# Kernel optimization log

Measured on AMD Instinct MI355X. Metric: run time of the kernel, lower is better.

The kernel has to match this reference:

```python
import jax, jax.numpy as jnp
import numpy as np

KE = 14.3996
ALPHA = 0.3
CUTOFF = 10.0
K_MAX = 6
N_ATOMS = 100000
N_PAIRS = 6400000
N_MOL = 64


def _generate_kvecs():
    kr = np.arange(0, K_MAX + 1, dtype=np.float32)
    kr = np.concatenate([kr, -kr[1:]])
    # cartesian product of (kr, kr, kr)
    g = np.stack(np.meshgrid(kr, kr, kr, indexing='ij'), axis=-1).reshape(-1, 3)
    norm = (g ** 2).sum(axis=1)
    mask = (norm <= K_MAX ** 2 + 2) & (norm != 0)
    return jnp.asarray(g[mask])  # [1020, 3]


def setup_inputs() -> dict:
    key = jax.random.key(0)
    k1, k2, k3, k4, k5, k6, k7 = jax.random.split(key, 7)
    partial_charges = jax.random.normal(k1, (N_ATOMS, 1), dtype=jnp.float32)
    # pair displacement vectors; scale so typical |r_ij| ~ 3-6 A, avoids d ~ 0
    Rij = jax.random.normal(k2, (N_PAIRS, 3), dtype=jnp.float32) * 3.0 + 1.0
    R = jax.random.uniform(k3, (N_ATOMS, 3), dtype=jnp.float32) * 20.0
    # orthorhombic-ish invertible cells: diag(~20) + small perturbation
    cell = jnp.eye(3, dtype=jnp.float32)[None] * 20.0 \
        + jax.random.uniform(k4, (N_MOL, 3, 3), dtype=jnp.float32) * 0.1
    idx_m = jnp.sort(jax.random.randint(k5, (N_ATOMS,), 0, N_MOL)).astype(jnp.int64)
    idx_i = jax.random.randint(k6, (N_PAIRS,), 0, N_ATOMS).astype(jnp.int64)
    idx_j = jax.random.randint(k7, (N_PAIRS,), 0, N_ATOMS).astype(jnp.int64)
    kvecs = _generate_kvecs()
    return {"partial_charges": partial_charges, "Rij": Rij, "R": R, "cell": cell,
            "kvecs": kvecs, "idx_m": idx_m, "idx_i": idx_i, "idx_j": idx_j}


def reference(partial_charges, Rij, R, cell, kvecs, idx_m, idx_i, idx_j):
    q = partial_charges.squeeze(-1)                      # [A]
    d_ij = jnp.linalg.norm(Rij, axis=1)                  # [P]
    sqrt_a = jnp.sqrt(jnp.float32(ALPHA))

    # ---- real space: gather q, erfc-screened pair potential, double scatter ----
    f_r = jax.scipy.special.erfc(sqrt_a * d_ij) / d_ij
    f_r_cut = jax.scipy.special.erfc(sqrt_a * CUTOFF) / CUTOFF
    pot_ij = q[idx_i] * q[idx_j] * (f_r - f_r_cut)
    pot_ij = jnp.where(d_ij <= CUTOFF, pot_ij, jnp.zeros_like(pot_ij))
    y_atom = jax.ops.segment_sum(pot_ij, idx_i, num_segments=N_ATOMS)
    y_real = 0.5 * KE * jax.ops.segment_sum(y_atom, idx_m, num_segments=N_MOL)

    # ---- reciprocal space ----
    two_pi = 2.0 * jnp.float32(np.pi)
    recip_box = two_pi * jnp.transpose(jnp.linalg.inv(cell), (0, 2, 1))  # [M,3,3]
    v_box = jnp.abs(jnp.linalg.det(cell))                                # [M]
    prefactor = two_pi / v_box
    kv = jnp.einsum('kd,mde->mke', kvecs, recip_box)     # [M,K,3]
    k_sq = jnp.sum(kv ** 2, axis=2)                      # [M,K]
    q_gauss = jnp.exp(-0.25 * k_sq / ALPHA)              # [M,K]
    # per-atom phase: gather per-molecule k-vectors, dot with positions
    kdp = jnp.einsum('akd,ad->ak', kv[idx_m], R)         # [A,K]
    q_real = jax.ops.segment_sum(q[:, None] * jnp.cos(kdp), idx_m, num_segments=N_MOL)
    q_imag = jax.ops.segment_sum(q[:, None] * jnp.sin(kdp), idx_m, num_segments=N_MOL)
    q_dens = q_real ** 2 + q_imag ** 2                   # [M,K]
    y_ewald = prefactor * jnp.sum(q_dens * q_gauss / k_sq, axis=1)
    self_int = jnp.sqrt(ALPHA / np.pi) * jax.ops.segment_sum(q ** 2, idx_m, num_segments=N_MOL)
    y_recip = KE * (y_ewald - self_int)

    return y_real + y_recip                              # [M]
```

## Files before the change

kernel.cpp:

```cpp
#include <hip/hip_runtime.h>
#include <math.h>

#define KE_C     14.3996f
#define ALPHA_C  0.3f
#define CUTOFF_C 10.0f
#define TWO_PI_C 6.283185307179586f
#define INV_2PI  0.15915494309189535f
#define ASPL     32
#define NK2      512

typedef float vfloat4 __attribute__((ext_vector_type(4)));
typedef int   vint4   __attribute__((ext_vector_type(4)));

__device__ __forceinline__ float fast_erfc(float x) {
    float t = __builtin_amdgcn_rcpf(fmaf(0.3275911f, x, 1.0f));
    float p = fmaf(t, 1.061405429f, -1.453152027f);
    p = fmaf(t, p, 1.421413741f);
    p = fmaf(t, p, -0.284496736f);
    p = fmaf(t, p, 0.254829592f);
    return t * p * __expf(-x * x);
}

__device__ __forceinline__ void sincos_rev(float x, float* s, float* c) {
    float f = __builtin_amdgcn_fractf(x);
    *s = __builtin_amdgcn_sinf(f);
    *c = __builtin_amdgcn_cosf(f);
}

__global__ __launch_bounds__(64) void k_cell(const float* __restrict__ cell,
                                             float* __restrict__ RB,
                                             float* __restrict__ VB, int nmol) {
    int m = blockIdx.x * blockDim.x + threadIdx.x;
    if (m >= nmol) return;
    const float* c = cell + m * 9;
    float a00 = c[0], a01 = c[1], a02 = c[2];
    float a10 = c[3], a11 = c[4], a12 = c[5];
    float a20 = c[6], a21 = c[7], a22 = c[8];
    float det = a00 * (a11 * a22 - a12 * a21)
              - a01 * (a10 * a22 - a12 * a20)
              + a02 * (a10 * a21 - a11 * a20);
    float id = 1.0f / det;
    float inv00 = (a11 * a22 - a12 * a21) * id;
    float inv01 = (a02 * a21 - a01 * a22) * id;
    float inv02 = (a01 * a12 - a02 * a11) * id;
    float inv10 = (a12 * a20 - a10 * a22) * id;
    float inv11 = (a00 * a22 - a02 * a20) * id;
    float inv12 = (a02 * a10 - a00 * a12) * id;
    float inv20 = (a10 * a21 - a11 * a20) * id;
    float inv21 = (a01 * a20 - a00 * a21) * id;
    float inv22 = (a00 * a11 - a01 * a10) * id;
    float* rb = RB + m * 9;
    rb[0] = TWO_PI_C * inv00; rb[1] = TWO_PI_C * inv10; rb[2] = TWO_PI_C * inv20;
    rb[3] = TWO_PI_C * inv01; rb[4] = TWO_PI_C * inv11; rb[5] = TWO_PI_C * inv21;
    rb[6] = TWO_PI_C * inv02; rb[7] = TWO_PI_C * inv12; rb[8] = TWO_PI_C * inv22;
    VB[m] = fabsf(det);
}

__global__ __launch_bounds__(128) void k_bounds(const int* __restrict__ idx_m,
                                                int* __restrict__ bounds,
                                                int natoms, int nmol) {
    int m = threadIdx.x;
    if (m > nmol) return;
    int lo = 0, hi = natoms;
    while (lo < hi) {
        int mid = (lo + hi) >> 1;
        if (idx_m[mid] < m) lo = mid + 1; else hi = mid;
    }
    bounds[m] = lo;
}

__global__ __launch_bounds__(256) void k_khalf(const float* __restrict__ kvecs,
                                               float4* __restrict__ KH,
                                               int* __restrict__ cnt, int nk) {
    int k = blockIdx.x * 256 + threadIdx.x;
    if (k >= nk) return;
    float gx = kvecs[3 * k], gy = kvecs[3 * k + 1], gz = kvecs[3 * k + 2];
    bool pos = (gx > 0.5f) ||
               (fabsf(gx) < 0.5f && (gy > 0.5f ||
                (fabsf(gy) < 0.5f && gz > 0.5f)));
    if (pos) {
        int s = atomicAdd(cnt, 1);
        KH[s] = make_float4(gx, gy, gz, 0.0f);
    }
}

__global__ __launch_bounds__(256) void k_atoms(const float* __restrict__ R,
                                               const float* __restrict__ q,
                                               const int* __restrict__ idx_m,
                                               const float* __restrict__ RB,
                                               float4* __restrict__ S4,
                                               float2* __restrict__ QM,
                                               float* __restrict__ SI, int natoms) {
    __shared__ float si[64];
    int tid = threadIdx.x;
    if (tid < 64) si[tid] = 0.0f;
    __syncthreads();
    int a = blockIdx.x * 256 + tid;
    if (a < natoms) {
        int m = idx_m[a];
        float r0 = R[3 * a], r1 = R[3 * a + 1], r2 = R[3 * a + 2];
        const float* rb = RB + m * 9;
        float s0 = (rb[0] * r0 + rb[1] * r1 + rb[2] * r2) * INV_2PI;
        float s1 = (rb[3] * r0 + rb[4] * r1 + rb[5] * r2) * INV_2PI;
        float s2 = (rb[6] * r0 + rb[7] * r1 + rb[8] * r2) * INV_2PI;
        float qa = q[a];
        S4[a] = make_float4(s0, s1, s2, qa);
        QM[a] = make_float2(qa, __int_as_float(m));
        atomicAdd(&si[m & 63], qa * qa);
    }
    __syncthreads();
    if (tid < 64) atomicAdd(&SI[tid], si[tid]);
}

__global__ __launch_bounds__(256) void k_main(const float4* __restrict__ S4,
                                              const float4* __restrict__ KH,
                                              const int* __restrict__ bounds,
                                              float* __restrict__ QR,
                                              float* __restrict__ QI, int nrecip,
                                              const float* __restrict__ Rij,
                                              const int* __restrict__ idx_i,
                                              const int* __restrict__ idx_j,
                                              const float2* __restrict__ QM,
                                              float* __restrict__ YRpad, int npairs) {
    __shared__ float acc[4][64];
    int tid = threadIdx.x;
    int bid = blockIdx.x;

    if (bid < nrecip) {
        int m  = bid / ASPL;
        int ac = bid % ASPL;
        int s0 = bounds[m], s1 = bounds[m + 1];
        int per = (s1 - s0 + ASPL - 1) / ASPL;
        int a0 = s0 + ac * per;
        int a1 = min(a0 + per, s1);
        float4 g0 = KH[tid];
        float4 g1 = KH[tid + 256];
        float qr0 = 0.f, qi0 = 0.f, qr1 = 0.f, qi1 = 0.f;
#pragma unroll 4
        for (int t = a0; t < a1; ++t) {
            float4 s = S4[t];
            float ph0 = fmaf(g0.x, s.x, fmaf(g0.y, s.y, g0.z * s.z));
            float ph1 = fmaf(g1.x, s.x, fmaf(g1.y, s.y, g1.z * s.z));
            float sn0, cs0, sn1, cs1;
            sincos_rev(ph0, &sn0, &cs0);
            sincos_rev(ph1, &sn1, &cs1);
            qr0 = fmaf(s.w, cs0, qr0);
            qi0 = fmaf(s.w, sn0, qi0);
            qr1 = fmaf(s.w, cs1, qr1);
            qi1 = fmaf(s.w, sn1, qi1);
        }
        atomicAdd(&QR[m * NK2 + tid], qr0);
        atomicAdd(&QI[m * NK2 + tid], qi0);
        atomicAdd(&QR[m * NK2 + tid + 256], qr1);
        atomicAdd(&QI[m * NK2 + tid + 256], qi1);
    } else {
        int wave = tid >> 6;
        ((float*)acc)[tid] = 0.0f;
        __syncthreads();
        const float sqa = 0.5477225575051661f;
        const float frcut = fast_erfc(sqa * CUTOFF_C) / CUTOFF_C;
        long base = ((long)(bid - nrecip) * 256 + tid) << 3;
        if (base + 8 <= npairs) {
            vint4 ii0 = __builtin_nontemporal_load((const vint4*)(idx_i + base));
            vint4 ii1 = __builtin_nontemporal_load((const vint4*)(idx_i + base) + 1);
            vint4 jj0 = __builtin_nontemporal_load((const vint4*)(idx_j + base));
            vint4 jj1 = __builtin_nontemporal_load((const vint4*)(idx_j + base) + 1);
            const vfloat4* r4 = (const vfloat4*)(Rij + 3 * base);
            vfloat4 A = __builtin_nontemporal_load(r4 + 0);
            vfloat4 B = __builtin_nontemporal_load(r4 + 1);
            vfloat4 C = __builtin_nontemporal_load(r4 + 2);
            vfloat4 D = __builtin_nontemporal_load(r4 + 3);
            vfloat4 E = __builtin_nontemporal_load(r4 + 4);
            vfloat4 F = __builtin_nontemporal_load(r4 + 5);
            float2 qa0 = QM[ii0.x], qa1 = QM[ii0.y], qa2 = QM[ii0.z], qa3 = QM[ii0.w];
            float2 qa4 = QM[ii1.x], qa5 = QM[ii1.y], qa6 = QM[ii1.z], qa7 = QM[ii1.w];
            float2 qb0 = QM[jj0.x], qb1 = QM[jj0.y], qb2 = QM[jj0.z], qb3 = QM[jj0.w];
            float2 qb4 = QM[jj1.x], qb5 = QM[jj1.y], qb6 = QM[jj1.z], qb7 = QM[jj1.w];
#define PAIR(xx, yy, zz, qa, qb)                                              \
            {                                                                 \
                float d2 = fmaf(xx, xx, fmaf(yy, yy, (zz) * (zz)));           \
                if (d2 <= CUTOFF_C * CUTOFF_C) {                              \
                    float rd = __builtin_amdgcn_rsqf(d2);                     \
                    float d = d2 * rd;                                        \
                    float f = fast_erfc(sqa * d) * rd - frcut;                \
                    atomicAdd(&acc[wave][__float_as_int((qa).y) & 63],        \
                              (qa).x * (qb).x * f);                           \
                }                                                             \
            }
            PAIR(A.x, A.y, A.z, qa0, qb0)
            PAIR(A.w, B.x, B.y, qa1, qb1)
            PAIR(B.z, B.w, C.x, qa2, qb2)
            PAIR(C.y, C.z, C.w, qa3, qb3)
            PAIR(D.x, D.y, D.z, qa4, qb4)
            PAIR(D.w, E.x, E.y, qa5, qb5)
            PAIR(E.z, E.w, F.x, qa6, qb6)
            PAIR(F.y, F.z, F.w, qa7, qb7)
#undef PAIR
        } else if (base < npairs) {
            for (long p = base; p < npairs; ++p) {
                float x = Rij[3 * p], y = Rij[3 * p + 1], z = Rij[3 * p + 2];
                float d2 = fmaf(x, x, fmaf(y, y, z * z));
                if (d2 <= CUTOFF_C * CUTOFF_C) {
                    float rd = __builtin_amdgcn_rsqf(d2);
                    float d = d2 * rd;
                    float2 qi2 = QM[idx_i[p]];
                    float2 qj2 = QM[idx_j[p]];
                    atomicAdd(&acc[wave][__float_as_int(qi2.y) & 63],
                              qi2.x * qj2.x * (fast_erfc(sqa * d) * rd - frcut));
                }
            }
        }
        __syncthreads();
        if (tid < 64) {
            float v = acc[0][tid] + acc[1][tid] + acc[2][tid] + acc[3][tid];
            atomicAdd(&YRpad[tid * 16], v);
        }
    }
}

__global__ __launch_bounds__(256) void k_final(const float4* __restrict__ KH,
                                               const int* __restrict__ cnt,
                                               const float* __restrict__ RB,
                                               const float* __restrict__ VB,
                                               const float* __restrict__ QR,
                                               const float* __restrict__ QI,
                                               const float* __restrict__ YRpad,
                                               const float* __restrict__ SI,
                                               float* __restrict__ out) {
    int m = blockIdx.x;
    int tid = threadIdx.x;
    __shared__ float rb[9];
    __shared__ float wsum[4];
    if (tid < 9) rb[tid] = RB[m * 9 + tid];
    __syncthreads();
    int nhalf = cnt[0];
    float acc = 0.0f;
    for (int k = tid; k < nhalf; k += 256) {
        float4 g = KH[k];
        float kv0 = g.x * rb[0] + g.y * rb[3] + g.z * rb[6];
        float kv1 = g.x * rb[1] + g.y * rb[4] + g.z * rb[7];
        float kv2 = g.x * rb[2] + g.y * rb[5] + g.z * rb[8];
        float ksq = kv0 * kv0 + kv1 * kv1 + kv2 * kv2;
        float qr = QR[m * NK2 + k], qi = QI[m * NK2 + k];
        acc += (qr * qr + qi * qi) * __expf(-0.25f / ALPHA_C * ksq) / ksq;
    }
#pragma unroll
    for (int off = 32; off > 0; off >>= 1) acc += __shfl_down(acc, off, 64);
    if ((tid & 63) == 0) wsum[tid >> 6] = acc;
    __syncthreads();
    if (tid == 0) {
        float s = 2.0f * (wsum[0] + wsum[1] + wsum[2] + wsum[3]);
        float pref = TWO_PI_C / VB[m];
        float self_c = sqrtf(ALPHA_C / 3.14159265358979323846f);
        out[m] = 0.5f * KE_C * YRpad[m * 16] + KE_C * (pref * s - self_c * SI[m]);
    }
}

extern "C" void kernel_launch(void* const* d_in, const int* in_sizes, int n_in,
                              void* d_out, int out_size, void* d_ws, size_t ws_size,
                              hipStream_t stream) {
    const float* q     = (const float*)d_in[0];
    const float* Rij   = (const float*)d_in[1];
    const float* R     = (const float*)d_in[2];
    const float* cell  = (const float*)d_in[3];
    const float* kvecs = (const float*)d_in[4];
    const int*   idx_m = (const int*)d_in[5];
    const int*   idx_i = (const int*)d_in[6];
    const int*   idx_j = (const int*)d_in[7];

    int natoms = in_sizes[0];
    int npairs = in_sizes[1] / 3;
    int nmol   = in_sizes[3] / 9;
    int nk     = in_sizes[4] / 3;
    float* out = (float*)d_out;

    float*  W      = (float*)d_ws;
    float*  RB     = W;
    float*  VB     = RB + 576;
    int*    bounds = (int*)(VB + 64);
    float4* S4     = (float4*)(W + 720);
    float2* QM     = (float2*)(W + 720 + 4 * (size_t)natoms);
    size_t  zoff   = 720 + 6 * (size_t)natoms;
    zoff = (zoff + 3) & ~(size_t)3;
    float4* KH     = (float4*)(W + zoff);
    float*  QR     = W + zoff + 4 * NK2;
    float*  QI     = QR + (size_t)nmol * NK2;
    float*  SI     = QI + (size_t)nmol * NK2;
    float*  YRpad  = SI + 64;
    int*    cnt    = (int*)(YRpad + 64 * 16);
    size_t zero_bytes = (4 * NK2 + (size_t)2 * nmol * NK2 + 64 + 64 * 16 + 4) * sizeof(float);
    (void)hipMemsetAsync(KH, 0, zero_bytes, stream);

    int nrecip = nmol * ASPL;
    int nrb = (npairs + 2047) / 2048;
    k_cell  <<<1, 64, 0, stream>>>(cell, RB, VB, nmol);
    k_bounds<<<1, 128, 0, stream>>>(idx_m, bounds, natoms, nmol);
    k_khalf <<<(nk + 255) / 256, 256, 0, stream>>>(kvecs, KH, cnt, nk);
    k_atoms <<<(natoms + 255) / 256, 256, 0, stream>>>(R, q, idx_m, RB, S4, QM, SI, natoms);
    k_main  <<<nrecip + nrb, 256, 0, stream>>>(S4, KH, bounds, QR, QI, nrecip,
                                               Rij, idx_i, idx_j, QM, YRpad, npairs);
    k_final <<<nmol, 256, 0, stream>>>(KH, cnt, RB, VB, QR, QI, YRpad, SI, out);
}
```

Before: 261.6 us.

## Pack charge and molecule id into one word, grid-stride real-space pair loop

Per-atom charge and molecule index are now packed into a single 32-bit word, with the molecule id in the low 6 mantissa bits. This halves the size of the gathered table and the bytes fetched per random gather. The real-space pair path becomes a persistent grid-stride loop over 2048 blocks, processing 4 pairs per iteration with regular loads instead of nontemporal ones. The cutoff branch is replaced by a select. Truncating the charge mantissa adds a small precision loss, and the fixed block count changes occupancy and tail behaviour.

```diff
diff --git a/kernel.cpp b/kernel.cpp
--- a/kernel.cpp
+++ b/kernel.cpp
@@ -8,6 +8,7 @@
 #define INV_2PI  0.15915494309189535f
 #define ASPL     32
 #define NK2      512
+#define NREAL    2048
 
 typedef float vfloat4 __attribute__((ext_vector_type(4)));
 typedef int   vint4   __attribute__((ext_vector_type(4)));
@@ -89,7 +90,7 @@
                                                const int* __restrict__ idx_m,
                                                const float* __restrict__ RB,
                                                float4* __restrict__ S4,
-                                               float2* __restrict__ QM,
+                                               unsigned int* __restrict__ QP,
                                                float* __restrict__ SI, int natoms) {
     __shared__ float si[64];
     int tid = threadIdx.x;
@@ -105,7 +106,7 @@
         float s2 = (rb[6] * r0 + rb[7] * r1 + rb[8] * r2) * INV_2PI;
         float qa = q[a];
         S4[a] = make_float4(s0, s1, s2, qa);
-        QM[a] = make_float2(qa, __int_as_float(m));
+        QP[a] = (__float_as_uint(qa) & ~63u) | (unsigned int)(m & 63);
         atomicAdd(&si[m & 63], qa * qa);
     }
     __syncthreads();
@@ -120,7 +121,7 @@
                                               const float* __restrict__ Rij,
                                               const int* __restrict__ idx_i,
                                               const int* __restrict__ idx_j,
-                                              const float2* __restrict__ QM,
+                                              const unsigned int* __restrict__ QP,
                                               float* __restrict__ YRpad, int npairs) {
     __shared__ float acc[4][64];
     int tid = threadIdx.x;
@@ -159,54 +160,45 @@
         __syncthreads();
         const float sqa = 0.5477225575051661f;
         const float frcut = fast_erfc(sqa * CUTOFF_C) / CUTOFF_C;
-        long base = ((long)(bid - nrecip) * 256 + tid) << 3;
-        if (base + 8 <= npairs) {
-            vint4 ii0 = __builtin_nontemporal_load((const vint4*)(idx_i + base));
-            vint4 ii1 = __builtin_nontemporal_load((const vint4*)(idx_i + base) + 1);
-            vint4 jj0 = __builtin_nontemporal_load((const vint4*)(idx_j + base));
-            vint4 jj1 = __builtin_nontemporal_load((const vint4*)(idx_j + base) + 1);
-            const vfloat4* r4 = (const vfloat4*)(Rij + 3 * base);
-            vfloat4 A = __builtin_nontemporal_load(r4 + 0);
-            vfloat4 B = __builtin_nontemporal_load(r4 + 1);
-            vfloat4 C = __builtin_nontemporal_load(r4 + 2);
-            vfloat4 D = __builtin_nontemporal_load(r4 + 3);
-            vfloat4 E = __builtin_nontemporal_load(r4 + 4);
-            vfloat4 F = __builtin_nontemporal_load(r4 + 5);
-            float2 qa0 = QM[ii0.x], qa1 = QM[ii0.y], qa2 = QM[ii0.z], qa3 = QM[ii0.w];
-            float2 qa4 = QM[ii1.x], qa5 = QM[ii1.y], qa6 = QM[ii1.z], qa7 = QM[ii1.w];
-            float2 qb0 = QM[jj0.x], qb1 = QM[jj0.y], qb2 = QM[jj0.z], qb3 = QM[jj0.w];
-            float2 qb4 = QM[jj1.x], qb5 = QM[jj1.y], qb6 = QM[jj1.z], qb7 = QM[jj1.w];
-#define PAIR(xx, yy, zz, qa, qb)                                              \
+        int nchunk = npairs >> 2;
+        int stride = NREAL * 256;
+        for (int c = (bid - nrecip) * 256 + tid; c < nchunk; c += stride) {
+            int p = c << 2;
+            vint4 ii = *(const vint4*)(idx_i + p);
+            vint4 jj = *(const vint4*)(idx_j + p);
+            const vfloat4* r4 = (const vfloat4*)(Rij + 3 * p);
+            vfloat4 A = r4[0], B = r4[1], C = r4[2];
+            unsigned int ui0 = QP[ii.x], ui1 = QP[ii.y], ui2 = QP[ii.z], ui3 = QP[ii.w];
+            unsigned int uj0 = QP[jj.x], uj1 = QP[jj.y], uj2 = QP[jj.z], uj3 = QP[jj.w];
+#define PAIR(xx, yy, zz, ui, uj)                                              \
             {                                                                 \
                 float d2 = fmaf(xx, xx, fmaf(yy, yy, (zz) * (zz)));           \
-                if (d2 <= CUTOFF_C * CUTOFF_C) {                              \
-                    float rd = __builtin_amdgcn_rsqf(d2);                     \
-                    float d = d2 * rd;                                        \
-                    float f = fast_erfc(sqa * d) * rd - frcut;                \
-                    atomicAdd(&acc[wave][__float_as_int((qa).y) & 63],        \
-                              (qa).x * (qb).x * f);                           \
-                }                                                             \
+                float rd = __builtin_amdgcn_rsqf(d2);                         \
+                float d = d2 * rd;                                            \
+                float f = fast_erfc(sqa * d) * rd - frcut;                    \
+                f = (d2 <= CUTOFF_C * CUTOFF_C) ? f : 0.0f;                   \
+                float qi_ = __uint_as_float((ui) & ~63u);                     \
+                float qj_ = __uint_as_float((uj) & ~63u);                     \
+                atomicAdd(&acc[wave][(ui) & 63u], qi_ * qj_ * f);             \
             }
-            PAIR(A.x, A.y, A.z, qa0, qb0)
-            PAIR(A.w, B.x, B.y, qa1, qb1)
-            PAIR(B.z, B.w, C.x, qa2, qb2)
-            PAIR(C.y, C.z, C.w, qa3, qb3)
-            PAIR(D.x, D.y, D.z, qa4, qb4)
-            PAIR(D.w, E.x, E.y, qa5, qb5)
-            PAIR(E.z, E.w, F.x, qa6, qb6)
-            PAIR(F.y, F.z, F.w, qa7, qb7)
+            PAIR(A.x, A.y, A.z, ui0, uj0)
+            PAIR(A.w, B.x, B.y, ui1, uj1)
+            PAIR(B.z, B.w, C.x, ui2, uj2)
+            PAIR(C.y, C.z, C.w, ui3, uj3)
 #undef PAIR
-        } else if (base < npairs) {
-            for (long p = base; p < npairs; ++p) {
+        }
+        if (bid == nrecip && tid == 0) {
+            for (int p = (npairs >> 2) << 2; p < npairs; ++p) {
                 float x = Rij[3 * p], y = Rij[3 * p + 1], z = Rij[3 * p + 2];
                 float d2 = fmaf(x, x, fmaf(y, y, z * z));
                 if (d2 <= CUTOFF_C * CUTOFF_C) {
                     float rd = __builtin_amdgcn_rsqf(d2);
                     float d = d2 * rd;
-                    float2 qi2 = QM[idx_i[p]];
-                    float2 qj2 = QM[idx_j[p]];
-                    atomicAdd(&acc[wave][__float_as_int(qi2.y) & 63],
-                              qi2.x * qj2.x * (fast_erfc(sqa * d) * rd - frcut));
+                    unsigned int ui = QP[idx_i[p]], uj = QP[idx_j[p]];
+                    float qi_ = __uint_as_float(ui & ~63u);
+                    float qj_ = __uint_as_float(uj & ~63u);
+                    atomicAdd(&acc[0][ui & 63u],
+                              qi_ * qj_ * (fast_erfc(sqa * d) * rd - frcut));
                 }
             }
         }
@@ -279,8 +271,8 @@
     float*  VB     = RB + 576;
     int*    bounds = (int*)(VB + 64);
     float4* S4     = (float4*)(W + 720);
-    float2* QM     = (float2*)(W + 720 + 4 * (size_t)natoms);
-    size_t  zoff   = 720 + 6 * (size_t)natoms;
+    unsigned int* QP = (unsigned int*)(W + 720 + 4 * (size_t)natoms);
+    size_t  zoff   = 720 + 5 * (size_t)natoms;
     zoff = (zoff + 3) & ~(size_t)3;
     float4* KH     = (float4*)(W + zoff);
     float*  QR     = W + zoff + 4 * NK2;
@@ -292,12 +284,11 @@
     (void)hipMemsetAsync(KH, 0, zero_bytes, stream);
 
     int nrecip = nmol * ASPL;
-    int nrb = (npairs + 2047) / 2048;
     k_cell  <<<1, 64, 0, stream>>>(cell, RB, VB, nmol);
     k_bounds<<<1, 128, 0, stream>>>(idx_m, bounds, natoms, nmol);
     k_khalf <<<(nk + 255) / 256, 256, 0, stream>>>(kvecs, KH, cnt, nk);
-    k_atoms <<<(natoms + 255) / 256, 256, 0, stream>>>(R, q, idx_m, RB, S4, QM, SI, natoms);
-    k_main  <<<nrecip + nrb, 256, 0, stream>>>(S4, KH, bounds, QR, QI, nrecip,
-                                               Rij, idx_i, idx_j, QM, YRpad, npairs);
+    k_atoms <<<(natoms + 255) / 256, 256, 0, stream>>>(R, q, idx_m, RB, S4, QP, SI, natoms);
+    k_main  <<<nrecip + NREAL, 256, 0, stream>>>(S4, KH, bounds, QR, QI, nrecip,
+                                                 Rij, idx_i, idx_j, QP, YRpad, npairs);
     k_final <<<nmol, 256, 0, stream>>>(KH, cnt, RB, VB, QR, QI, YRpad, SI, out);
 }
```

Measured after the change: 247.1 us. -5.5%, faster.
